# Kernel tuning notes

Hardware: AMD Instinct MI355X
Metric: run time of the kernel (lower is better)

The kernel has to match this reference:

```python
import jax, jax.numpy as jnp
import numpy as np

N_NODES = 100000
N_EDGES = 1600000
NUM_RELS = 8
IN_FEAT = 128
OUT_FEAT = 128


def setup_inputs() -> dict:
    key = jax.random.key(0)
    k1, k2, k3, k4, k5 = jax.random.split(key, 5)
    feat = jax.random.normal(k1, (N_NODES, IN_FEAT), dtype=jnp.float32)
    weight = jax.random.normal(k2, (NUM_RELS, IN_FEAT, OUT_FEAT), dtype=jnp.float32) * 0.05
    src = jax.random.randint(k3, (N_EDGES,), 0, N_NODES, dtype=jnp.int64 if jax.config.jax_enable_x64 else jnp.int32)
    dst = jax.random.randint(k4, (N_EDGES,), 0, N_NODES, dtype=jnp.int64 if jax.config.jax_enable_x64 else jnp.int32)
    etypes = jax.random.randint(k5, (N_EDGES,), 0, NUM_RELS, dtype=jnp.int64 if jax.config.jax_enable_x64 else jnp.int32)
    return {"feat": feat, "weight": weight, "src": src, "dst": dst, "etypes": etypes}


def reference(feat, weight, src, dst, etypes):
    # RGCN segment_mm: per edge e, message m_e = feat[src[e]] @ weight[etypes[e]],
    # then sum-aggregate messages into destination nodes.
    # The torch module sorts edges by etype only so segment_mm can run a grouped
    # GEMM; the scatter-sum aggregation is order-independent, so sorting does not
    # change the math. We compute all per-relation projections densely (small R)
    # and gather the right one per edge -- equivalent math, fully vectorized.
    proj = jnp.einsum('ni,rio->rno', feat, weight)      # [R, N, out]
    m = proj[etypes, src]                               # [E, out] gather per edge
    out = jax.ops.segment_sum(m, dst, num_segments=feat.shape[0])  # [N, out]
    return out
```

## Files before the change

kernel.cpp:

```cpp
#include <hip/hip_runtime.h>
#include <hip/hip_bf16.h>


#define FEAT 128
#define SCAN_BLK 1024
#define LDKB 136

typedef __attribute__((ext_vector_type(8))) short short8;
typedef __attribute__((ext_vector_type(8))) __bf16 bf16x8;
typedef __attribute__((ext_vector_type(4))) float f32x4;

__device__ __forceinline__ unsigned f2bf(float x) {
    union { float f; unsigned u; } v; v.f = x;
    unsigned r = v.u + 0x7FFFu + ((v.u >> 16) & 1u);
    return r >> 16;
}

__global__ void cvt_feat_kernel(const float* __restrict__ f,
                                ushort* __restrict__ o, int n8) {
    int i = blockIdx.x * blockDim.x + threadIdx.x;
    if (i >= n8) return;
    const float4* f4 = (const float4*)f;
    float4 a = f4[2 * i], b = f4[2 * i + 1];
    union { ushort u[8]; int4 v; } pk;
    pk.u[0] = f2bf(a.x); pk.u[1] = f2bf(a.y); pk.u[2] = f2bf(a.z); pk.u[3] = f2bf(a.w);
    pk.u[4] = f2bf(b.x); pk.u[5] = f2bf(b.y); pk.u[6] = f2bf(b.z); pk.u[7] = f2bf(b.w);
    ((int4*)o)[i] = pk.v;
}

__global__ void cvt_w_kernel(const float* __restrict__ w,
                             ushort* __restrict__ wt, int total, int KW) {
    int i = blockIdx.x * blockDim.x + threadIdx.x;
    if (i >= total) return;
    int n = i / KW;
    int rk = i - n * KW;
    int r = rk >> 7, k = rk & 127;
    wt[i] = (ushort)f2bf(w[(r << 14) + (k << 7) + n]);
}

__global__ void hist_kernel(const int* __restrict__ dst,
                            const int* __restrict__ et, int E, int R,
                            int* __restrict__ cnt) {
    int i = blockIdx.x * blockDim.x + threadIdx.x;
    int stride = gridDim.x * blockDim.x;
    for (; i < E; i += stride) atomicAdd(&cnt[dst[i] * R + et[i]], 1);
}

__global__ void scan1_kernel(const int* __restrict__ cnt, int* __restrict__ bsum) {
    int lane = threadIdx.x;
    int base = blockIdx.x * SCAN_BLK + lane * 16;
    int s = 0;
    #pragma unroll
    for (int i = 0; i < 16; i++) s += cnt[base + i];
    for (int o = 32; o; o >>= 1) s += __shfl_down(s, o, 64);
    if (lane == 0) bsum[blockIdx.x] = s;
}

__global__ void scan2_kernel(int* __restrict__ bsum, int nb) {
    __shared__ int tmp[SCAN_BLK];
    int t = threadIdx.x;
    int v = (t < nb) ? bsum[t] : 0;
    tmp[t] = v;
    __syncthreads();
    for (int o = 1; o < SCAN_BLK; o <<= 1) {
        int x = (t >= o) ? tmp[t - o] : 0;
        __syncthreads();
        tmp[t] += x;
        __syncthreads();
    }
    if (t < nb) bsum[t] = tmp[t] - v;
}

__global__ void scan3_kernel(const int* __restrict__ cnt,
                             const int* __restrict__ bsum,
                             int* __restrict__ off, int* __restrict__ cursor) {
    int lane = threadIdx.x;
    int base = blockIdx.x * SCAN_BLK + lane * 16;
    int local[16]; int s = 0;
    #pragma unroll
    for (int i = 0; i < 16; i++) { local[i] = cnt[base + i]; s += local[i]; }
    int x = s;
    for (int o = 1; o < 64; o <<= 1) { int y = __shfl_up(x, o, 64); if (lane >= o) x += y; }
    int run = bsum[blockIdx.x] + x - s;
    #pragma unroll
    for (int i = 0; i < 16; i++) { off[base + i] = run; cursor[base + i] = run; run += local[i]; }
}

__global__ void scatter_kernel(const int* __restrict__ dst,
                               const int* __restrict__ et,
                               const int* __restrict__ src, int E, int R,
                               int* __restrict__ cursor, int* __restrict__ sidx) {
    int i = blockIdx.x * blockDim.x + threadIdx.x;
    int stride = gridDim.x * blockDim.x;
    for (; i < E; i += stride) {
        int p = atomicAdd(&cursor[dst[i] * R + et[i]], 1);
        sidx[p] = src[i];
    }
}

__global__ __launch_bounds__(256, 3)
void fused_kernel(const ushort* __restrict__ featb,
                  const ushort* __restrict__ wtb,
                  const int* __restrict__ sidx, const int* __restrict__ off,
                  float* __restrict__ out, int N, int R, int KW) {
    __shared__ __align__(16) ushort Ssm[128 * LDKB];
    int t = threadIdx.x, wid = t >> 6, lane = t & 63;
    int eq = lane >> 4, c = lane & 15;
    int lm = lane & 15, lq = lane >> 4;
    int base = blockIdx.x * 128;
    int mq = (wid >> 1) * 64, nq = (wid & 1) * 64;

    f32x4 acc[16];
    #pragma unroll
    for (int i = 0; i < 16; i++) acc[i] = (f32x4){0.f, 0.f, 0.f, 0.f};

    for (int r = 0; r < R; r++) {
        #pragma unroll 2
        for (int g = 0; g < 8; g++) {
            int dl = g * 16 + wid * 4 + eq;
            int d = base + dl;
            int beg = 0, end = 0;
            if (d < N) {
                beg = off[d * R + r];
                end = off[d * R + r + 1];
            }
            float a[8];
            #pragma unroll
            for (int i = 0; i < 8; i++) a[i] = 0.f;
            for (int pos = beg; pos < end; pos += 4) {
                int sv[4];
                #pragma unroll
                for (int jj = 0; jj < 4; jj++) {
                    int p = pos + jj;
                    sv[jj] = (p < end) ? sidx[p] : -1;
                }
                #pragma unroll
                for (int jj = 0; jj < 4; jj++) {
                    if (sv[jj] >= 0) {
                        uint4 v = *(const uint4*)(featb + (size_t)sv[jj] * FEAT + c * 8);
                        a[0] += __uint_as_float(v.x << 16);
                        a[1] += __uint_as_float(v.x & 0xffff0000u);
                        a[2] += __uint_as_float(v.y << 16);
                        a[3] += __uint_as_float(v.y & 0xffff0000u);
                        a[4] += __uint_as_float(v.z << 16);
                        a[5] += __uint_as_float(v.z & 0xffff0000u);
                        a[6] += __uint_as_float(v.w << 16);
                        a[7] += __uint_as_float(v.w & 0xffff0000u);
                    }
                }
            }
            uint4 pk;
            pk.x = f2bf(a[0]) | (f2bf(a[1]) << 16);
            pk.y = f2bf(a[2]) | (f2bf(a[3]) << 16);
            pk.z = f2bf(a[4]) | (f2bf(a[5]) << 16);
            pk.w = f2bf(a[6]) | (f2bf(a[7]) << 16);
            *(uint4*)&Ssm[dl * LDKB + c * 8] = pk;
        }
        __syncthreads();

        const ushort* bp = wtb + (size_t)(nq + lm) * KW + r * FEAT;
        #pragma unroll
        for (int ks = 0; ks < 4; ks++) {
            int kof = ks * 32 + lq * 8;
            short8 af[4], bfg[4];
            #pragma unroll
            for (int tm = 0; tm < 4; tm++)
                af[tm] = *(const short8*)&Ssm[(mq + tm * 16 + lm) * LDKB + kof];
            #pragma unroll
            for (int tn = 0; tn < 4; tn++)
                bfg[tn] = *(const short8*)(bp + (size_t)(tn * 16) * KW + kof);
            #pragma unroll
            for (int tm = 0; tm < 4; tm++)
                #pragma unroll
                for (int tn = 0; tn < 4; tn++)
                    acc[tm * 4 + tn] = __builtin_amdgcn_mfma_f32_16x16x32_bf16(
                        __builtin_bit_cast(bf16x8, af[tm]),
                        __builtin_bit_cast(bf16x8, bfg[tn]),
                        acc[tm * 4 + tn], 0, 0, 0);
        }
        __syncthreads();
    }

    #pragma unroll
    for (int tm = 0; tm < 4; tm++) {
        #pragma unroll
        for (int i = 0; i < 4; i++) {
            int row = base + mq + tm * 16 + lq * 4 + i;
            if (row < N) {
                float* op = out + (size_t)row * FEAT + nq + lm;
                #pragma unroll
                for (int tn = 0; tn < 4; tn++) op[tn * 16] = acc[tm * 4 + tn][i];
            }
        }
    }
}

static inline size_t al256(size_t x) { return (x + 255) & ~(size_t)255; }

extern "C" void kernel_launch(void* const* d_in, const int* in_sizes, int n_in,
                              void* d_out, int out_size, void* d_ws,
                              size_t ws_size, hipStream_t stream) {
    const float* feat = (const float*)d_in[0];
    const float* weight = (const float*)d_in[1];
    const int* src = (const int*)d_in[2];
    const int* dst = (const int*)d_in[3];
    const int* et = (const int*)d_in[4];

    int nfeat = in_sizes[0];
    int N = nfeat / FEAT;
    int R = in_sizes[1] / (FEAT * FEAT);
    int E = in_sizes[2];
    int Npad = ((N + 127) / 128) * 128;
    int KW = R * FEAT;
    float* out = (float*)d_out;

    int nkeys_raw = N * R + 1;
    int KEYS = ((nkeys_raw + SCAN_BLK - 1) / SCAN_BLK) * SCAN_BLK;
    int nb = KEYS / SCAN_BLK;

    char* ws = (char*)d_ws;
    size_t o = 0;
    size_t cnt_o  = o; o += al256((size_t)KEYS * 4);
    size_t bsum_o = o; o += al256((size_t)SCAN_BLK * 4);
    size_t off_o  = o; o += al256((size_t)KEYS * 4);
    size_t cur_o  = o; o += al256((size_t)KEYS * 4);
    size_t sidx_o = o; o += al256((size_t)E * 4);
    size_t wtb_o  = o; o += al256((size_t)R * FEAT * FEAT * 2);
    size_t featb_o = o;

    int* cnt    = (int*)(ws + cnt_o);
    int* bsum   = (int*)(ws + bsum_o);
    int* off    = (int*)(ws + off_o);
    int* cursor = (int*)(ws + cur_o);
    int* sidx   = (int*)(ws + sidx_o);
    ushort* wtb   = (ushort*)(ws + wtb_o);
    ushort* featb = (ushort*)(ws + featb_o);

    hipMemsetAsync(cnt, 0, (size_t)KEYS * 4, stream);

    int wtotal = R * FEAT * FEAT;
    cvt_w_kernel<<<(wtotal + 255) / 256, 256, 0, stream>>>(weight, wtb, wtotal, KW);
    int n8 = nfeat / 8;
    cvt_feat_kernel<<<(n8 + 255) / 256, 256, 0, stream>>>(feat, featb, n8);

    hist_kernel<<<784, 256, 0, stream>>>(dst, et, E, R, cnt);
    scan1_kernel<<<nb, 64, 0, stream>>>(cnt, bsum);
    scan2_kernel<<<1, SCAN_BLK, 0, stream>>>(bsum, nb);
    scan3_kernel<<<nb, 64, 0, stream>>>(cnt, bsum, off, cursor);
    scatter_kernel<<<784, 256, 0, stream>>>(dst, et, src, E, R, cursor, sidx);

    fused_kernel<<<Npad / 128, 256, 0, stream>>>(featb, wtb, sidx, off,
                                                 out, N, R, KW);
}
```

Baseline: 523.5 us.

## Replace CSR sort with fixed-capacity block buckets and LDS atomic aggregation

Removes the histogram and three-pass scan used to build a per-(node, relation) CSR. A single scatter pass now writes packed (src, local dst) records into fixed-capacity buckets keyed by (128-node block, relation). The fused kernel zeroes an fp32 shared tile per relation and accumulates gathered features into it with LDS float atomics, then converts to bf16 when loading MFMA operands. This cuts launches and preprocessing traffic and evens out per-lane work, at the cost of shared-memory atomic contention, a larger shared tile with lower occupancy (launch bounds 3 to 2), and silently dropping edges if any bucket exceeds CAP.

```diff
diff --git a/kernel.cpp b/kernel.cpp
--- a/kernel.cpp
+++ b/kernel.cpp
@@ -3,8 +3,8 @@
 
 
 #define FEAT 128
-#define SCAN_BLK 1024
-#define LDKB 136
+#define LDW 132
+#define CAP 1024
 
 typedef __attribute__((ext_vector_type(8))) short short8;
 typedef __attribute__((ext_vector_type(8))) __bf16 bf16x8;
@@ -14,6 +14,12 @@
     union { float f; unsigned u; } v; v.f = x;
     unsigned r = v.u + 0x7FFFu + ((v.u >> 16) & 1u);
     return r >> 16;
+}
+
+__device__ __forceinline__ unsigned pkbf(float lo, float hi) {
+    unsigned ul = __float_as_uint(lo) + 0x8000u;
+    unsigned uh = __float_as_uint(hi) + 0x8000u;
+    return (uh & 0xffff0000u) | (ul >> 16);
 }
 
 __global__ void cvt_feat_kernel(const float* __restrict__ f,
@@ -38,123 +44,79 @@
     wt[i] = (ushort)f2bf(w[(r << 14) + (k << 7) + n]);
 }
 
-__global__ void hist_kernel(const int* __restrict__ dst,
-                            const int* __restrict__ et, int E, int R,
-                            int* __restrict__ cnt) {
-    int i = blockIdx.x * blockDim.x + threadIdx.x;
-    int stride = gridDim.x * blockDim.x;
-    for (; i < E; i += stride) atomicAdd(&cnt[dst[i] * R + et[i]], 1);
-}
-
-__global__ void scan1_kernel(const int* __restrict__ cnt, int* __restrict__ bsum) {
-    int lane = threadIdx.x;
-    int base = blockIdx.x * SCAN_BLK + lane * 16;
-    int s = 0;
-    #pragma unroll
-    for (int i = 0; i < 16; i++) s += cnt[base + i];
-    for (int o = 32; o; o >>= 1) s += __shfl_down(s, o, 64);
-    if (lane == 0) bsum[blockIdx.x] = s;
-}
-
-__global__ void scan2_kernel(int* __restrict__ bsum, int nb) {
-    __shared__ int tmp[SCAN_BLK];
-    int t = threadIdx.x;
-    int v = (t < nb) ? bsum[t] : 0;
-    tmp[t] = v;
-    __syncthreads();
-    for (int o = 1; o < SCAN_BLK; o <<= 1) {
-        int x = (t >= o) ? tmp[t - o] : 0;
-        __syncthreads();
-        tmp[t] += x;
-        __syncthreads();
-    }
-    if (t < nb) bsum[t] = tmp[t] - v;
-}
-
-__global__ void scan3_kernel(const int* __restrict__ cnt,
-                             const int* __restrict__ bsum,
-                             int* __restrict__ off, int* __restrict__ cursor) {
-    int lane = threadIdx.x;
-    int base = blockIdx.x * SCAN_BLK + lane * 16;
-    int local[16]; int s = 0;
-    #pragma unroll
-    for (int i = 0; i < 16; i++) { local[i] = cnt[base + i]; s += local[i]; }
-    int x = s;
-    for (int o = 1; o < 64; o <<= 1) { int y = __shfl_up(x, o, 64); if (lane >= o) x += y; }
-    int run = bsum[blockIdx.x] + x - s;
-    #pragma unroll
-    for (int i = 0; i < 16; i++) { off[base + i] = run; cursor[base + i] = run; run += local[i]; }
-}
-
 __global__ void scatter_kernel(const int* __restrict__ dst,
                                const int* __restrict__ et,
                                const int* __restrict__ src, int E, int R,
-                               int* __restrict__ cursor, int* __restrict__ sidx) {
+                               int sbits, int* __restrict__ cursor,
+                               int* __restrict__ recs) {
     int i = blockIdx.x * blockDim.x + threadIdx.x;
     int stride = gridDim.x * blockDim.x;
     for (; i < E; i += stride) {
-        int p = atomicAdd(&cursor[dst[i] * R + et[i]], 1);
-        sidx[p] = src[i];
+        int d = dst[i];
+        int b = (d >> 7) * R + et[i];
+        int p = atomicAdd(&cursor[b], 1);
+        if (p < CAP) recs[(size_t)b * CAP + p] = src[i] | ((d & 127) << sbits);
     }
 }
 
-__global__ __launch_bounds__(256, 3)
+__global__ __launch_bounds__(256, 2)
 void fused_kernel(const ushort* __restrict__ featb,
                   const ushort* __restrict__ wtb,
-                  const int* __restrict__ sidx, const int* __restrict__ off,
-                  float* __restrict__ out, int N, int R, int KW) {
-    __shared__ __align__(16) ushort Ssm[128 * LDKB];
+                  const int* __restrict__ recs,
+                  const int* __restrict__ cursor,
+                  float* __restrict__ out, int N, int R, int KW, int sbits) {
+    __shared__ __align__(16) float Sf[128 * LDW];
     int t = threadIdx.x, wid = t >> 6, lane = t & 63;
     int eq = lane >> 4, c = lane & 15;
     int lm = lane & 15, lq = lane >> 4;
-    int base = blockIdx.x * 128;
+    int blk = blockIdx.x, base = blk * 128;
     int mq = (wid >> 1) * 64, nq = (wid & 1) * 64;
+    int qid = wid * 4 + eq;
+    int smask = (1 << sbits) - 1;
 
     f32x4 acc[16];
     #pragma unroll
     for (int i = 0; i < 16; i++) acc[i] = (f32x4){0.f, 0.f, 0.f, 0.f};
 
     for (int r = 0; r < R; r++) {
-        #pragma unroll 2
-        for (int g = 0; g < 8; g++) {
-            int dl = g * 16 + wid * 4 + eq;
-            int d = base + dl;
-            int beg = 0, end = 0;
-            if (d < N) {
-                beg = off[d * R + r];
-                end = off[d * R + r + 1];
-            }
-            float a[8];
-            #pragma unroll
-            for (int i = 0; i < 8; i++) a[i] = 0.f;
-            for (int pos = beg; pos < end; pos += 4) {
-                int sv[4];
-                #pragma unroll
-                for (int jj = 0; jj < 4; jj++) {
-                    int p = pos + jj;
-                    sv[jj] = (p < end) ? sidx[p] : -1;
+        int bkt = blk * R + r;
+        int ecnt = cursor[bkt];
+        if (ecnt <= 0) continue;
+        if (ecnt > CAP) ecnt = CAP;
+
+        #pragma unroll 4
+        for (int i = t; i < 128 * LDW / 4; i += 256)
+            ((float4*)Sf)[i] = (float4){0.f, 0.f, 0.f, 0.f};
+        __syncthreads();
+
+        const int* rb = recs + (size_t)bkt * CAP;
+        for (int e0 = 0; e0 < ecnt; e0 += 64) {
+            int rv[4]; uint4 v[4];
+            #pragma unroll
+            for (int u = 0; u < 4; u++) {
+                int idx = e0 + u * 16 + qid;
+                rv[u] = (idx < ecnt) ? rb[idx] : -1;
+            }
+            #pragma unroll
+            for (int u = 0; u < 4; u++)
+                if (rv[u] >= 0)
+                    v[u] = *(const uint4*)(featb +
+                           (size_t)(rv[u] & smask) * FEAT + c * 8);
+            #pragma unroll
+            for (int u = 0; u < 4; u++) {
+                if (rv[u] >= 0) {
+                    int dl = (rv[u] >> sbits) & 127;
+                    float* sp = &Sf[dl * LDW + c * 8];
+                    atomicAdd(sp + 0, __uint_as_float(v[u].x << 16));
+                    atomicAdd(sp + 1, __uint_as_float(v[u].x & 0xffff0000u));
+                    atomicAdd(sp + 2, __uint_as_float(v[u].y << 16));
+                    atomicAdd(sp + 3, __uint_as_float(v[u].y & 0xffff0000u));
+                    atomicAdd(sp + 4, __uint_as_float(v[u].z << 16));
+                    atomicAdd(sp + 5, __uint_as_float(v[u].z & 0xffff0000u));
+                    atomicAdd(sp + 6, __uint_as_float(v[u].w << 16));
+                    atomicAdd(sp + 7, __uint_as_float(v[u].w & 0xffff0000u));
                 }
-                #pragma unroll
-                for (int jj = 0; jj < 4; jj++) {
-                    if (sv[jj] >= 0) {
-                        uint4 v = *(const uint4*)(featb + (size_t)sv[jj] * FEAT + c * 8);
-                        a[0] += __uint_as_float(v.x << 16);
-                        a[1] += __uint_as_float(v.x & 0xffff0000u);
-                        a[2] += __uint_as_float(v.y << 16);
-                        a[3] += __uint_as_float(v.y & 0xffff0000u);
-                        a[4] += __uint_as_float(v.z << 16);
-                        a[5] += __uint_as_float(v.z & 0xffff0000u);
-                        a[6] += __uint_as_float(v.w << 16);
-                        a[7] += __uint_as_float(v.w & 0xffff0000u);
-                    }
-                }
-            }
-            uint4 pk;
-            pk.x = f2bf(a[0]) | (f2bf(a[1]) << 16);
-            pk.y = f2bf(a[2]) | (f2bf(a[3]) << 16);
-            pk.z = f2bf(a[4]) | (f2bf(a[5]) << 16);
-            pk.w = f2bf(a[6]) | (f2bf(a[7]) << 16);
-            *(uint4*)&Ssm[dl * LDKB + c * 8] = pk;
+            }
         }
         __syncthreads();
 
@@ -164,8 +126,17 @@
             int kof = ks * 32 + lq * 8;
             short8 af[4], bfg[4];
             #pragma unroll
-            for (int tm = 0; tm < 4; tm++)
-                af[tm] = *(const short8*)&Ssm[(mq + tm * 16 + lm) * LDKB + kof];
+            for (int tm = 0; tm < 4; tm++) {
+                const float* sp = &Sf[(mq + tm * 16 + lm) * LDW + kof];
+                f32x4 x = *(const f32x4*)sp;
+                f32x4 y = *(const f32x4*)(sp + 4);
+                union { unsigned u[4]; short8 s; } pk;
+                pk.u[0] = pkbf(x[0], x[1]);
+                pk.u[1] = pkbf(x[2], x[3]);
+                pk.u[2] = pkbf(y[0], y[1]);
+                pk.u[3] = pkbf(y[2], y[3]);
+                af[tm] = pk.s;
+            }
             #pragma unroll
             for (int tn = 0; tn < 4; tn++)
                 bfg[tn] = *(const short8*)(bp + (size_t)(tn * 16) * KW + kof);
@@ -211,44 +182,36 @@
     int R = in_sizes[1] / (FEAT * FEAT);
     int E = in_sizes[2];
     int Npad = ((N + 127) / 128) * 128;
+    int nblk = Npad / 128;
+    int NB = nblk * R;
     int KW = R * FEAT;
     float* out = (float*)d_out;
 
-    int nkeys_raw = N * R + 1;
-    int KEYS = ((nkeys_raw + SCAN_BLK - 1) / SCAN_BLK) * SCAN_BLK;
-    int nb = KEYS / SCAN_BLK;
+    int sbits = 1;
+    while ((1 << sbits) < N) sbits++;
 
     char* ws = (char*)d_ws;
     size_t o = 0;
-    size_t cnt_o  = o; o += al256((size_t)KEYS * 4);
-    size_t bsum_o = o; o += al256((size_t)SCAN_BLK * 4);
-    size_t off_o  = o; o += al256((size_t)KEYS * 4);
-    size_t cur_o  = o; o += al256((size_t)KEYS * 4);
-    size_t sidx_o = o; o += al256((size_t)E * 4);
+    size_t cur_o  = o; o += al256((size_t)NB * 4);
+    size_t recs_o = o; o += al256((size_t)NB * CAP * 4);
     size_t wtb_o  = o; o += al256((size_t)R * FEAT * FEAT * 2);
     size_t featb_o = o;
 
-    int* cnt    = (int*)(ws + cnt_o);
-    int* bsum   = (int*)(ws + bsum_o);
-    int* off    = (int*)(ws + off_o);
     int* cursor = (int*)(ws + cur_o);
-    int* sidx   = (int*)(ws + sidx_o);
+    int* recs   = (int*)(ws + recs_o);
     ushort* wtb   = (ushort*)(ws + wtb_o);
     ushort* featb = (ushort*)(ws + featb_o);
 
-    hipMemsetAsync(cnt, 0, (size_t)KEYS * 4, stream);
+    hipMemsetAsync(cursor, 0, (size_t)NB * 4, stream);
 
     int wtotal = R * FEAT * FEAT;
     cvt_w_kernel<<<(wtotal + 255) / 256, 256, 0, stream>>>(weight, wtb, wtotal, KW);
     int n8 = nfeat / 8;
     cvt_feat_kernel<<<(n8 + 255) / 256, 256, 0, stream>>>(feat, featb, n8);
 
-    hist_kernel<<<784, 256, 0, stream>>>(dst, et, E, R, cnt);
-    scan1_kernel<<<nb, 64, 0, stream>>>(cnt, bsum);
-    scan2_kernel<<<1, SCAN_BLK, 0, stream>>>(bsum, nb);
-    scan3_kernel<<<nb, 64, 0, stream>>>(cnt, bsum, off, cursor);
-    scatter_kernel<<<784, 256, 0, stream>>>(dst, et, src, E, R, cursor, sidx);
-
-    fused_kernel<<<Npad / 128, 256, 0, stream>>>(featb, wtb, sidx, off,
-                                                 out, N, R, KW);
-}
+    scatter_kernel<<<512, 256, 0, stream>>>(dst, et, src, E, R, sbits,
+                                            cursor, recs);
+
+    fused_kernel<<<nblk, 256, 0, stream>>>(featb, wtb, recs, cursor,
+                                           out, N, R, KW, sbits);
+}
```

New measurement: 1.571 ms. 200% more time.
